# Kernel optimization log

Measured on AMD Instinct MI355X. Metric: run time of the kernel, lower is better.

Reference implementation:

```python
import jax, jax.numpy as jnp
import numpy as np

IN_F = 2048
OUT_F = 2048
BATCH = 16384
BASE_SPARSITY = 0.02
REVIVAL_DENSITY = 0.2   # rows for dead ('low') output neurons
RELIEF_DENSITY = 0.15   # cols for saturated ('high') input neurons
DEAD = np.arange(16)                      # 'low' extrema (row indices)
SATURATED = np.arange(100, 900, 100)      # 'high' extrema (col indices)


def _make_mask(key):
    k1, k2, k3 = jax.random.split(key, 3)
    base = (jax.random.uniform(k1, (OUT_F, IN_F)) < BASE_SPARSITY).astype(jnp.float32)
    patch = jnp.zeros((OUT_F, IN_F), jnp.float32)
    # dense-ish rows for dead output neurons
    row_patch = (jax.random.uniform(k2, (len(DEAD), IN_F)) < REVIVAL_DENSITY).astype(jnp.float32)
    patch = patch.at[jnp.asarray(DEAD), :].set(row_patch)
    # dense-ish cols for saturated input neurons (overwrite, matching torch order)
    col_patch = (jax.random.uniform(k3, (OUT_F, len(SATURATED))) < RELIEF_DENSITY).astype(jnp.float32)
    patch = patch.at[:, jnp.asarray(SATURATED)].set(col_patch)
    return jnp.maximum(base, patch)


def setup_inputs() -> dict:
    key = jax.random.key(0)
    kx, kw, km = jax.random.split(key, 3)
    x = jax.random.normal(kx, (BATCH, IN_F), dtype=jnp.float32)
    # kaiming_uniform_(a=sqrt(5)) -> U(-bound, bound), bound = sqrt(6/((1+a^2)*fan_in)) = 1/sqrt(fan_in)
    bound = 1.0 / np.sqrt(IN_F)
    weight = jax.random.uniform(kw, (OUT_F, IN_F), minval=-bound, maxval=bound, dtype=jnp.float32)
    bias = jnp.zeros((OUT_F,), jnp.float32)
    mask = _make_mask(km)
    return {"x": x, "weight": weight, "bias": bias, "mask": mask}


def reference(x, weight, bias, mask):
    # F.linear(x, weight * mask, bias): y = x @ (W*M)^T + b
    return jnp.einsum('bi,oi->bo', x, weight * mask) + bias
```

## Files before the change

kernel.cpp:

```cpp
#include <hip/hip_runtime.h>
#include <stdint.h>

#define BATCH 16384
#define IN_F 2048
#define OUT_F 2048

typedef unsigned short u16;
typedef __attribute__((ext_vector_type(8))) short bf16x8;
typedef __attribute__((ext_vector_type(4))) float f32x4;

__device__ __forceinline__ u16 f2bf(float f) {
  union { float f; uint32_t u; } v; v.f = f;
  uint32_t u = v.u;
  u += 0x7FFFu + ((u >> 16) & 1u);
  return (u16)(u >> 16);
}


__global__ void cvt_x_kernel(const float4* __restrict__ x, u16* __restrict__ out) {
  int i = blockIdx.x * 256 + threadIdx.x;
  float4 v = x[i];
  uint2 p;
  p.x = (uint32_t)f2bf(v.x) | ((uint32_t)f2bf(v.y) << 16);
  p.y = (uint32_t)f2bf(v.z) | ((uint32_t)f2bf(v.w) << 16);
  ((uint2*)out)[i] = p;
}

__global__ void cvt_w_kernel(const float4* __restrict__ w, const float4* __restrict__ m,
                             u16* __restrict__ out) {
  int i = blockIdx.x * 256 + threadIdx.x;
  float4 wv = w[i];
  float4 mv = m[i];
  uint2 p;
  p.x = (uint32_t)f2bf(wv.x * mv.x) | ((uint32_t)f2bf(wv.y * mv.y) << 16);
  p.y = (uint32_t)f2bf(wv.z * mv.z) | ((uint32_t)f2bf(wv.w * mv.w) << 16);
  ((uint2*)out)[i] = p;
}


__device__ __forceinline__ void async_cp16(const void* g, void* l) {
  __builtin_amdgcn_global_load_lds(
      (const __attribute__((address_space(1))) void*)g,
      (__attribute__((address_space(3))) void*)l,
      16, 0, 0);
}


__global__ __launch_bounds__(256) void gemm_bf16(const u16* __restrict__ A,
                                                 const u16* __restrict__ B,
                                                 const float* __restrict__ bias,
                                                 float* __restrict__ C) {
  __shared__ u16 lsA[128 * 32];
  __shared__ u16 lsB[128 * 32];
  const int K = IN_F, N = OUT_F;
  const int tid = threadIdx.x;
  const int lane = tid & 63, wave = tid >> 6;
  const int waveM = (wave & 1) * 64, waveN = (wave >> 1) * 64;
  const long bm = (long)blockIdx.x * 128;
  const long bn = (long)blockIdx.y * 128;

  const int o1 = tid * 16;
  const int o2 = o1 + 4096;
  const int r1 = tid >> 2, r2 = r1 + 64;
  const int c = tid & 3;
  const int cs1 = c ^ ((r1 >> 1) & 3);
  const int cs2 = c ^ ((r2 >> 1) & 3);
  const u16* gA1 = A + (bm + r1) * K + cs1 * 8;
  const u16* gA2 = A + (bm + r2) * K + cs2 * 8;
  const u16* gB1 = B + (bn + r1) * K + cs1 * 8;
  const u16* gB2 = B + (bn + r2) * K + cs2 * 8;
  char* lA1 = (char*)lsA + o1;
  char* lA2 = (char*)lsA + o2;
  char* lB1 = (char*)lsB + o1;
  char* lB2 = (char*)lsB + o2;

  f32x4 acc[4][4];
#pragma unroll
  for (int i = 0; i < 4; i++)
#pragma unroll
    for (int j = 0; j < 4; j++)
#pragma unroll
      for (int r = 0; r < 4; r++) acc[i][j][r] = 0.0f;

  const int mrow = lane & 15;
  const int q = lane >> 4;

  for (int k0 = 0; k0 < K; k0 += 32) {
    async_cp16(gA1 + k0, lA1);
    async_cp16(gA2 + k0, lA2);
    async_cp16(gB1 + k0, lB1);
    async_cp16(gB2 + k0, lB2);
    __syncthreads();

    bf16x8 af[4], bfr[4];
#pragma unroll
    for (int i = 0; i < 4; i++) {
      const int rr = waveM + i * 16 + mrow;
      af[i] = *(const bf16x8*)&lsA[rr * 32 + (q ^ ((rr >> 1) & 3)) * 8];
    }
#pragma unroll
    for (int j = 0; j < 4; j++) {
      const int rr = waveN + j * 16 + mrow;
      bfr[j] = *(const bf16x8*)&lsB[rr * 32 + (q ^ ((rr >> 1) & 3)) * 8];
    }

#pragma unroll
    for (int i = 0; i < 4; i++)
#pragma unroll
      for (int j = 0; j < 4; j++)
        acc[i][j] = __builtin_amdgcn_mfma_f32_16x16x32_bf16(af[i], bfr[j], acc[i][j], 0, 0, 0);

    __syncthreads();
  }

  const int cn = lane & 15;
  const int crow = (lane >> 4) * 4;
#pragma unroll
  for (int j = 0; j < 4; j++) {
    const long n = bn + waveN + j * 16 + cn;
    const float bv = bias[n];
#pragma unroll
    for (int i = 0; i < 4; i++) {
      const long m0 = bm + waveM + i * 16 + crow;
      float* cp = C + m0 * N + n;
#pragma unroll
      for (int r = 0; r < 4; r++)
        cp[(long)r * N] = acc[i][j][r] + bv;
    }
  }
}


__global__ void naive_kernel(const float* __restrict__ x, const float* __restrict__ w,
                             const float* __restrict__ bias, const float* __restrict__ m,
                             float* __restrict__ out) {
  size_t idx = (size_t)blockIdx.x * 256 + threadIdx.x;
  int o = (int)(idx % OUT_F);
  size_t b = idx / OUT_F;
  float s = bias[o];
  const float* xr = x + b * IN_F;
  const float* wr = w + (size_t)o * IN_F;
  const float* mr = m + (size_t)o * IN_F;
  for (int k = 0; k < IN_F; k++) s += xr[k] * wr[k] * mr[k];
  out[idx] = s;
}

extern "C" void kernel_launch(void* const* d_in, const int* in_sizes, int n_in,
                              void* d_out, int out_size, void* d_ws, size_t ws_size,
                              hipStream_t stream) {
  const float* x = (const float*)d_in[0];
  const float* w = (const float*)d_in[1];
  const float* bias = (const float*)d_in[2];
  const float* mask = (const float*)d_in[3];
  float* out = (float*)d_out;

  const size_t xb_elems = (size_t)BATCH * IN_F;
  const size_t wm_elems = (size_t)OUT_F * IN_F;
  const size_t need = (xb_elems + wm_elems) * sizeof(u16);

  if (ws_size >= need) {
    u16* xb = (u16*)d_ws;
    u16* wm = xb + xb_elems;
    cvt_x_kernel<<<(uint32_t)(xb_elems / 4 / 256), 256, 0, stream>>>((const float4*)x, xb);
    cvt_w_kernel<<<(uint32_t)(wm_elems / 4 / 256), 256, 0, stream>>>((const float4*)w,
                                                                     (const float4*)mask, wm);
    gemm_bf16<<<dim3(BATCH / 128, OUT_F / 128), 256, 0, stream>>>(xb, wm, bias, out);
  } else {
    naive_kernel<<<(uint32_t)(((size_t)BATCH * OUT_F) / 256), 256, 0, stream>>>(x, w, bias, mask, out);
  }
}
```

Measured before the change: 408.2 us.

## Use 256x256 tiles with a 4-stage async LDS pipeline and fused conversion

The bf16 GEMM moves from a 128x128 tile with 256 threads and a single-buffered LDS loop to a 256x256 tile with 512 threads. It uses a 4-slot circular LDS buffer filled by async global-to-LDS loads, with explicit vmcnt waits, barriers and setprio around the MFMA phases. The goal is to hide global-load latency and raise data reuse per tile. The x and weight*mask conversion kernels are also merged into one launch. In exchange the kernel needs 128 KB of LDS and many accumulator registers, which limits occupancy to roughly one block per CU.

```diff
diff --git a/kernel.cpp b/kernel.cpp
--- a/kernel.cpp
+++ b/kernel.cpp
@@ -17,24 +17,26 @@
 }
 
 
-__global__ void cvt_x_kernel(const float4* __restrict__ x, u16* __restrict__ out) {
+__global__ void cvt_fused(const float4* __restrict__ x, const float4* __restrict__ w,
+                          const float4* __restrict__ m, u16* __restrict__ xb,
+                          u16* __restrict__ wb) {
+  const int NX = BATCH * IN_F / 4;
   int i = blockIdx.x * 256 + threadIdx.x;
-  float4 v = x[i];
-  uint2 p;
-  p.x = (uint32_t)f2bf(v.x) | ((uint32_t)f2bf(v.y) << 16);
-  p.y = (uint32_t)f2bf(v.z) | ((uint32_t)f2bf(v.w) << 16);
-  ((uint2*)out)[i] = p;
-}
-
-__global__ void cvt_w_kernel(const float4* __restrict__ w, const float4* __restrict__ m,
-                             u16* __restrict__ out) {
-  int i = blockIdx.x * 256 + threadIdx.x;
-  float4 wv = w[i];
-  float4 mv = m[i];
-  uint2 p;
-  p.x = (uint32_t)f2bf(wv.x * mv.x) | ((uint32_t)f2bf(wv.y * mv.y) << 16);
-  p.y = (uint32_t)f2bf(wv.z * mv.z) | ((uint32_t)f2bf(wv.w * mv.w) << 16);
-  ((uint2*)out)[i] = p;
+  if (i < NX) {
+    float4 v = x[i];
+    uint2 p;
+    p.x = (uint32_t)f2bf(v.x) | ((uint32_t)f2bf(v.y) << 16);
+    p.y = (uint32_t)f2bf(v.z) | ((uint32_t)f2bf(v.w) << 16);
+    ((uint2*)xb)[i] = p;
+  } else {
+    int j = i - NX;
+    float4 wv = w[j];
+    float4 mv = m[j];
+    uint2 p;
+    p.x = (uint32_t)f2bf(wv.x * mv.x) | ((uint32_t)f2bf(wv.y * mv.y) << 16);
+    p.y = (uint32_t)f2bf(wv.z * mv.z) | ((uint32_t)f2bf(wv.w * mv.w) << 16);
+    ((uint2*)wb)[j] = p;
+  }
 }
 
 
@@ -46,82 +48,111 @@
 }
 
 
-__global__ __launch_bounds__(256) void gemm_bf16(const u16* __restrict__ A,
-                                                 const u16* __restrict__ B,
-                                                 const float* __restrict__ bias,
-                                                 float* __restrict__ C) {
-  __shared__ u16 lsA[128 * 32];
-  __shared__ u16 lsB[128 * 32];
+#define BK 32
+#define NT (IN_F / BK)
+
+__global__ __launch_bounds__(512, 2) void gemm_bf16(const u16* __restrict__ A,
+                                                    const u16* __restrict__ B,
+                                                    const float* __restrict__ bias,
+                                                    float* __restrict__ C) {
+  __shared__ __align__(128) char smem[4 * 32768];
   const int K = IN_F, N = OUT_F;
   const int tid = threadIdx.x;
   const int lane = tid & 63, wave = tid >> 6;
-  const int waveM = (wave & 1) * 64, waveN = (wave >> 1) * 64;
-  const long bm = (long)blockIdx.x * 128;
-  const long bn = (long)blockIdx.y * 128;
-
-  const int o1 = tid * 16;
-  const int o2 = o1 + 4096;
-  const int r1 = tid >> 2, r2 = r1 + 64;
-  const int c = tid & 3;
-  const int cs1 = c ^ ((r1 >> 1) & 3);
-  const int cs2 = c ^ ((r2 >> 1) & 3);
-  const u16* gA1 = A + (bm + r1) * K + cs1 * 8;
-  const u16* gA2 = A + (bm + r2) * K + cs2 * 8;
-  const u16* gB1 = B + (bn + r1) * K + cs1 * 8;
-  const u16* gB2 = B + (bn + r2) * K + cs2 * 8;
-  char* lA1 = (char*)lsA + o1;
-  char* lA2 = (char*)lsA + o2;
-  char* lB1 = (char*)lsB + o1;
-  char* lB2 = (char*)lsB + o2;
-
-  f32x4 acc[4][4];
-#pragma unroll
-  for (int i = 0; i < 4; i++)
+  const int wm = wave >> 2;
+  const int wn = wave & 3;
+  const long bn = (long)blockIdx.x * 256;
+  const long bm = (long)blockIdx.y * 256;
+
+  const int sr = tid >> 2, sc = tid & 3;
+  const int scs = sc ^ ((sr >> 1) & 3);
+  const u16* gA = A + (bm + sr) * K + scs * 8;
+  const u16* gB = B + (bn + sr) * K + scs * 8;
+  const long hiK = 128L * K;
+  const int ldst = tid * 16;
+
+  auto stageA = [&](int slot, int kt) {
+    char* sb = smem + slot * 32768;
+    const long ko = (long)kt * BK;
+    async_cp16(gA + ko, sb + ldst);
+    async_cp16(gA + hiK + ko, sb + 8192 + ldst);
+  };
+  auto stageB = [&](int slot, int kt) {
+    char* sb = smem + slot * 32768 + 16384;
+    const long ko = (long)kt * BK;
+    async_cp16(gB + ko, sb + ldst);
+    async_cp16(gB + hiK + ko, sb + 8192 + ldst);
+  };
+
+  const int rl = lane & 15;
+  const int q = lane >> 4;
+  const int fb = rl * 64 + ((q ^ ((rl >> 1) & 3)) * 16);
+
+  f32x4 acc[8][4];
+#pragma unroll
+  for (int i = 0; i < 8; i++)
 #pragma unroll
     for (int j = 0; j < 4; j++)
 #pragma unroll
       for (int r = 0; r < 4; r++) acc[i][j][r] = 0.0f;
 
-  const int mrow = lane & 15;
-  const int q = lane >> 4;
-
-  for (int k0 = 0; k0 < K; k0 += 32) {
-    async_cp16(gA1 + k0, lA1);
-    async_cp16(gA2 + k0, lA2);
-    async_cp16(gB1 + k0, lB1);
-    async_cp16(gB2 + k0, lB2);
-    __syncthreads();
-
-    bf16x8 af[4], bfr[4];
-#pragma unroll
-    for (int i = 0; i < 4; i++) {
-      const int rr = waveM + i * 16 + mrow;
-      af[i] = *(const bf16x8*)&lsA[rr * 32 + (q ^ ((rr >> 1) & 3)) * 8];
-    }
-#pragma unroll
-    for (int j = 0; j < 4; j++) {
-      const int rr = waveN + j * 16 + mrow;
-      bfr[j] = *(const bf16x8*)&lsB[rr * 32 + (q ^ ((rr >> 1) & 3)) * 8];
-    }
-
+  stageA(0, 0); stageB(0, 0);
+  stageA(1, 1); stageB(1, 1);
+  stageA(2, 2); stageB(2, 2);
+  asm volatile("s_waitcnt vmcnt(8)" ::: "memory");
+  __builtin_amdgcn_s_barrier();
+  __builtin_amdgcn_sched_barrier(0);
+
+  for (int t = 0; t < NT; ++t) {
+    const int slot = t & 3;
+    const int kt3 = (t + 3 < NT) ? t + 3 : NT - 1;
+    const int s3 = (t + 3) & 3;
+    const char* sA = smem + slot * 32768 + wm * 8192;
+    const char* sB = smem + slot * 32768 + 16384 + wn * 4096;
+
+    bf16x8 af0[4], af1[4], bf[4];
+#pragma unroll
+    for (int i = 0; i < 4; i++) af0[i] = *(const bf16x8*)(sA + i * 1024 + fb);
+#pragma unroll
+    for (int j = 0; j < 4; j++) bf[j] = *(const bf16x8*)(sB + j * 1024 + fb);
+    stageA(s3, kt3);
+    __builtin_amdgcn_s_barrier();
+    __builtin_amdgcn_s_setprio(1);
 #pragma unroll
     for (int i = 0; i < 4; i++)
 #pragma unroll
       for (int j = 0; j < 4; j++)
-        acc[i][j] = __builtin_amdgcn_mfma_f32_16x16x32_bf16(af[i], bfr[j], acc[i][j], 0, 0, 0);
-
-    __syncthreads();
-  }
+        acc[i][j] = __builtin_amdgcn_mfma_f32_16x16x32_bf16(af0[i], bf[j], acc[i][j], 0, 0, 0);
+    __builtin_amdgcn_s_setprio(0);
+    __builtin_amdgcn_s_barrier();
+
+#pragma unroll
+    for (int i = 0; i < 4; i++) af1[i] = *(const bf16x8*)(sA + 4096 + i * 1024 + fb);
+    stageB(s3, kt3);
+    __builtin_amdgcn_s_barrier();
+    __builtin_amdgcn_s_setprio(1);
+#pragma unroll
+    for (int i = 0; i < 4; i++)
+#pragma unroll
+      for (int j = 0; j < 4; j++)
+        acc[4 + i][j] = __builtin_amdgcn_mfma_f32_16x16x32_bf16(af1[i], bf[j], acc[4 + i][j], 0, 0, 0);
+    __builtin_amdgcn_s_setprio(0);
+    asm volatile("s_waitcnt vmcnt(8)" ::: "memory");
+    __builtin_amdgcn_s_barrier();
+    __builtin_amdgcn_sched_barrier(0);
+  }
+
+  asm volatile("s_waitcnt vmcnt(0)" ::: "memory");
 
   const int cn = lane & 15;
   const int crow = (lane >> 4) * 4;
 #pragma unroll
   for (int j = 0; j < 4; j++) {
-    const long n = bn + waveN + j * 16 + cn;
+    const long n = bn + wn * 64 + j * 16 + cn;
     const float bv = bias[n];
 #pragma unroll
-    for (int i = 0; i < 4; i++) {
-      const long m0 = bm + waveM + i * 16 + crow;
+    for (int i = 0; i < 8; i++) {
+      const long m0 = bm + wm * 128 + i * 16 + crow;
       float* cp = C + m0 * N + n;
 #pragma unroll
       for (int r = 0; r < 4; r++)
@@ -161,10 +192,10 @@
   if (ws_size >= need) {
     u16* xb = (u16*)d_ws;
     u16* wm = xb + xb_elems;
-    cvt_x_kernel<<<(uint32_t)(xb_elems / 4 / 256), 256, 0, stream>>>((const float4*)x, xb);
-    cvt_w_kernel<<<(uint32_t)(wm_elems / 4 / 256), 256, 0, stream>>>((const float4*)w,
-                                                                     (const float4*)mask, wm);
-    gemm_bf16<<<dim3(BATCH / 128, OUT_F / 128), 256, 0, stream>>>(xb, wm, bias, out);
+    const uint32_t nblk = (uint32_t)((xb_elems + wm_elems) / 4 / 256);
+    cvt_fused<<<nblk, 256, 0, stream>>>((const float4*)x, (const float4*)w,
+                                        (const float4*)mask, xb, wm);
+    gemm_bf16<<<dim3(OUT_F / 256, BATCH / 256), 512, 0, stream>>>(xb, wm, bias, out);
   } else {
     naive_kernel<<<(uint32_t)(((size_t)BATCH * OUT_F) / 256), 256, 0, stream>>>(x, w, bias, mask, out);
   }
```

Result: faster. 371.4 us (-9.0%).
